# Kernel optimization log

Measured on AMD Instinct MI355X. Metric: run time of the kernel, lower is better.

## Reference

```python
import jax, jax.numpy as jnp
import numpy as np

KERNEL_MUL = 2.0
KERNEL_NUM = 5

def setup_inputs() -> dict:
    key = jax.random.key(0)
    k1, k2 = jax.random.split(key)
    source = jax.random.normal(k1, (4096, 256), dtype=jnp.float32)
    target = jax.random.normal(k2, (4096, 256), dtype=jnp.float32)
    return {"source": source, "target": target}

def reference(source, target):
    B = source.shape[0]
    total = jnp.concatenate([source, target], axis=0)           # [2N, D]
    n = total.shape[0]
    # pairwise squared L2 distances via expansion (same math as
    # ((total0 - total1)**2).sum(2) without the [2N,2N,D] intermediate)
    sq = jnp.sum(total * total, axis=-1)                         # [2N]
    l2 = jnp.maximum(sq[:, None] + sq[None, :] - 2.0 * (total @ total.T), 0.0)  # [2N,2N]
    # bandwidth from data mean of off-diagonal distances (detached in torch via .data)
    bandwidth = jax.lax.stop_gradient(jnp.sum(l2)) / (n * n - n)
    bandwidth = bandwidth / (KERNEL_MUL ** (KERNEL_NUM // 2))
    kernels = jnp.zeros_like(l2)
    for i in range(KERNEL_NUM):
        kernels = kernels + jnp.exp(-l2 / (bandwidth * (KERNEL_MUL ** i)))
    xx = kernels[:B, :B]
    yy = kernels[B:, B:]
    xy = kernels[:B, B:]
    yx = kernels[B:, :B]
    return jnp.mean(xx + yy - xy - yx)
```

## Files before the change

kernel.cpp:

```cpp
#include <hip/hip_runtime.h>


#define NROWS 8192
#define BHALF 4096
#define DDIM  256
#define TILE  128
#define BK    32
#define NTILE 64
#define NBLK  2080

typedef __attribute__((ext_vector_type(8))) short bf16x8;
typedef __attribute__((ext_vector_type(4))) float f32x4;
typedef __attribute__((ext_vector_type(2))) float f32x2;
typedef __attribute__((ext_vector_type(4))) unsigned short u16x4;

struct Ws {
  float coef;
  float Spart[256];
  float cpart[256][256];
  float sq[NROWS];
  float part[NBLK];
};

__device__ __forceinline__ unsigned short f2bf(float x) {
  unsigned int u = __builtin_bit_cast(unsigned int, x);
  return (unsigned short)((u + 0x7fffu + ((u >> 16) & 1u)) >> 16);
}

__device__ __forceinline__ const float* row_ptr(const float* src, const float* tgt, int i) {
  return (i < BHALF) ? (src + (size_t)i * DDIM) : (tgt + (size_t)(i - BHALF) * DDIM);
}

__global__ __launch_bounds__(256) void k_prep(const float* __restrict__ src,
                                              const float* __restrict__ tgt,
                                              Ws* __restrict__ ws,
                                              unsigned short* __restrict__ tb,
                                              int conv) {
  __shared__ float cls[4][256];
  __shared__ float sred[4];
  int tid = threadIdx.x, wave = tid >> 6, lane = tid & 63;
  int row0 = blockIdx.x * 32 + wave * 8;
  float c0 = 0.f, c1 = 0.f, c2 = 0.f, c3 = 0.f;
  float s[8];
  #pragma unroll
  for (int r = 0; r < 8; ++r) {
    const float4* rp = (const float4*)row_ptr(src, tgt, row0 + r);
    float4 x = rp[lane];
    if (conv) {
      u16x4 b = { f2bf(x.x), f2bf(x.y), f2bf(x.z), f2bf(x.w) };
      int rg = row0 + r;
      int t = rg >> 7, rl = rg & 127;
      int cg = lane >> 1;
      int k8 = cg >> 2, cwp = cg & 3;
      int slot = cwp ^ ((rl >> 1) & 3);
      *(u16x4*)&tb[((size_t)(t * 8 + k8) * 128 + rl) * 32 + slot * 8 + (lane & 1) * 4] = b;
    }
    c0 += x.x; c1 += x.y; c2 += x.z; c3 += x.w;
    s[r] = x.x * x.x + x.y * x.y + x.z * x.z + x.w * x.w;
  }
  #pragma unroll
  for (int off = 32; off > 0; off >>= 1) {
    #pragma unroll
    for (int r = 0; r < 8; ++r) s[r] += __shfl_xor(s[r], off);
  }
  if (lane == 0) {
    float Sw = 0.f;
    #pragma unroll
    for (int r = 0; r < 8; ++r) { ws->sq[row0 + r] = s[r]; Sw += s[r]; }
    sred[wave] = Sw;
  }
  cls[wave][lane * 4 + 0] = c0;
  cls[wave][lane * 4 + 1] = c1;
  cls[wave][lane * 4 + 2] = c2;
  cls[wave][lane * 4 + 3] = c3;
  __syncthreads();
  ws->cpart[blockIdx.x][tid] = cls[0][tid] + cls[1][tid] + cls[2][tid] + cls[3][tid];
  if (tid == 0) ws->Spart[blockIdx.x] = sred[0] + sred[1] + sred[2] + sred[3];
}

__global__ __launch_bounds__(256) void k_bw(Ws* __restrict__ ws) {
  __shared__ float redm[4], reds[4];
  int tid = threadIdx.x, wave = tid >> 6, lane = tid & 63;
  float mc = 0.f;
  for (int b0 = 0; b0 < 256; b0 += 16) {
    float v[16];
    #pragma unroll
    for (int j = 0; j < 16; ++j) v[j] = ws->cpart[b0 + j][tid];
    #pragma unroll
    for (int j = 0; j < 16; ++j) mc += v[j];
  }
  float p = mc * mc;
  float sp = ws->Spart[tid];
  #pragma unroll
  for (int off = 32; off > 0; off >>= 1) {
    p  += __shfl_xor(p, off);
    sp += __shfl_xor(sp, off);
  }
  if (lane == 0) { redm[wave] = p; reds[wave] = sp; }
  __syncthreads();
  if (tid == 0) {
    float msq = redm[0] + redm[1] + redm[2] + redm[3];
    float S   = reds[0] + reds[1] + reds[2] + reds[3];
    double n = (double)NROWS;
    double sum_l2 = 2.0 * n * (double)S - 2.0 * (double)msq;
    double bw = sum_l2 / (n * n - n) / 4.0;
    ws->coef = (float)(1.4426950408889634 / (16.0 * bw));
  }
}

__device__ __forceinline__ void stage32(const unsigned short* gA,
                                        const unsigned short* gB,
                                        unsigned short* lA, unsigned short* lB,
                                        int kcs) {
  #pragma unroll
  for (int t = 0; t < 2; ++t) {
    __builtin_amdgcn_global_load_lds(
        (const __attribute__((address_space(1))) void*)(gA + (size_t)kcs * 4096 + t * 512),
        (__attribute__((address_space(3))) void*)(lA + t * 512), 16, 0, 0);
    __builtin_amdgcn_global_load_lds(
        (const __attribute__((address_space(1))) void*)(gB + (size_t)kcs * 4096 + t * 512),
        (__attribute__((address_space(3))) void*)(lB + t * 512), 16, 0, 0);
  }
}

template <int FAST>
__global__ __launch_bounds__(256, 4) void k_main(const unsigned short* __restrict__ tb,
                                                 const float* __restrict__ src,
                                                 const float* __restrict__ tgt,
                                                 Ws* __restrict__ ws) {
  int bid = blockIdx.x;
  int idx = (bid & 7) * (NBLK / 8) + (bid >> 3);
  int ti = (int)((129.0 - sqrt(129.0 * 129.0 - 8.0 * (double)idx)) * 0.5);
  while (64 * (ti + 1) - ((ti + 1) * ti) / 2 <= idx) ++ti;
  while (64 * ti - (ti * (ti - 1)) / 2 > idx) --ti;
  int tj = ti + (idx - (64 * ti - (ti * (ti - 1)) / 2));

  __shared__ __align__(16) unsigned short As[2][TILE * BK];
  __shared__ __align__(16) unsigned short Bs[2][TILE * BK];
  __shared__ float wsum[4];

  int tid = threadIdx.x;
  int wave = tid >> 6, lane = tid & 63;
  int wm = wave >> 1, wn = wave & 1;
  int lr = lane & 15, q = lane >> 4;
  int Ib = ti * TILE, Jb = tj * TILE;

  f32x4 zero = {0.f, 0.f, 0.f, 0.f};
  f32x4 acc[4][4];
  #pragma unroll
  for (int m = 0; m < 4; ++m)
    #pragma unroll
    for (int n = 0; n < 4; ++n) acc[m][n] = zero;

  const int coff = ((q ^ ((lr >> 1) & 3)) << 3);

  if (FAST) {
    const unsigned short* gA = tb + (size_t)ti * 32768 + wave * 1024 + lane * 8;
    const unsigned short* gB = tb + (size_t)tj * 32768 + wave * 1024 + lane * 8;
    unsigned short* lA0 = &As[0][wave * 1024];
    unsigned short* lB0 = &Bs[0][wave * 1024];
    unsigned short* lA1 = &As[1][wave * 1024];
    unsigned short* lB1 = &Bs[1][wave * 1024];

    stage32(gA, gB, lA0, lB0, 0);
    #pragma unroll
    for (int kcs = 0; kcs < 8; ++kcs) {
      if (kcs < 7) {
        stage32(gA, gB, ((kcs + 1) & 1) ? lA1 : lA0,
                        ((kcs + 1) & 1) ? lB1 : lB0, kcs + 1);
        asm volatile("s_waitcnt vmcnt(4)" ::: "memory");
      } else {
        asm volatile("s_waitcnt vmcnt(0)" ::: "memory");
      }
      __builtin_amdgcn_s_barrier();
      const unsigned short* Ab = As[kcs & 1];
      const unsigned short* Bb = Bs[kcs & 1];
      bf16x8 af[4], bfr[4];
      #pragma unroll
      for (int m = 0; m < 4; ++m)
        af[m] = *(const bf16x8*)&Ab[(wm * 64 + m * 16 + lr) * BK + coff];
      #pragma unroll
      for (int n = 0; n < 4; ++n)
        bfr[n] = *(const bf16x8*)&Bb[(wn * 64 + n * 16 + lr) * BK + coff];
      #pragma unroll
      for (int m = 0; m < 4; ++m)
        #pragma unroll
        for (int n = 0; n < 4; ++n)
          acc[m][n] = __builtin_amdgcn_mfma_f32_16x16x32_bf16(af[m], bfr[n], acc[m][n], 0, 0, 0);
      __builtin_amdgcn_s_barrier();
    }
  } else {
    int row = tid >> 1, h = tid & 1;
    int fsw = (row >> 1) & 3;
    const float4* rpA = (const float4*)row_ptr(src, tgt, Ib + row);
    const float4* rpB = (const float4*)row_ptr(src, tgt, Jb + row);
    #pragma unroll
    for (int kcs = 0; kcs < 8; ++kcs) {
      if (kcs) __syncthreads();
      unsigned short* lA = As[kcs & 1];
      unsigned short* lB = Bs[kcs & 1];
      #pragma unroll
      for (int cc = 0; cc < 2; ++cc) {
        int c = h * 2 + cc;
        int slot = c ^ fsw;
        float4 v0 = rpA[kcs * 8 + c * 2], v1 = rpA[kcs * 8 + c * 2 + 1];
        u16x4 a0 = { f2bf(v0.x), f2bf(v0.y), f2bf(v0.z), f2bf(v0.w) };
        u16x4 a1 = { f2bf(v1.x), f2bf(v1.y), f2bf(v1.z), f2bf(v1.w) };
        *(u16x4*)&lA[row * BK + slot * 8]     = a0;
        *(u16x4*)&lA[row * BK + slot * 8 + 4] = a1;
        float4 w0 = rpB[kcs * 8 + c * 2], w1 = rpB[kcs * 8 + c * 2 + 1];
        u16x4 b0 = { f2bf(w0.x), f2bf(w0.y), f2bf(w0.z), f2bf(w0.w) };
        u16x4 b1 = { f2bf(w1.x), f2bf(w1.y), f2bf(w1.z), f2bf(w1.w) };
        *(u16x4*)&lB[row * BK + slot * 8]     = b0;
        *(u16x4*)&lB[row * BK + slot * 8 + 4] = b1;
      }
      __syncthreads();
      const unsigned short* Ab = As[kcs & 1];
      const unsigned short* Bb = Bs[kcs & 1];
      bf16x8 af[4], bfr[4];
      #pragma unroll
      for (int m = 0; m < 4; ++m)
        af[m] = *(const bf16x8*)&Ab[(wm * 64 + m * 16 + lr) * BK + coff];
      #pragma unroll
      for (int n = 0; n < 4; ++n)
        bfr[n] = *(const bf16x8*)&Bb[(wn * 64 + n * 16 + lr) * BK + coff];
      #pragma unroll
      for (int m = 0; m < 4; ++m)
        #pragma unroll
        for (int n = 0; n < 4; ++n)
          acc[m][n] = __builtin_amdgcn_mfma_f32_16x16x32_bf16(af[m], bfr[n], acc[m][n], 0, 0, 0);
    }
  }

  float coef = ws->coef;
  float coef2 = 2.f * coef;
  int ibase = Ib + wm * 64;
  int jbase = Jb + wn * 64;
  float nscj[4];
  f32x2 nsci01[4], nsci23[4];
  #pragma unroll
  for (int n = 0; n < 4; ++n) nscj[n] = -ws->sq[jbase + n * 16 + lr] * coef;
  #pragma unroll
  for (int m = 0; m < 4; ++m) {
    nsci01[m] = f32x2{ -ws->sq[ibase + m * 16 + q * 4 + 0] * coef,
                       -ws->sq[ibase + m * 16 + q * 4 + 1] * coef };
    nsci23[m] = f32x2{ -ws->sq[ibase + m * 16 + q * 4 + 2] * coef,
                       -ws->sq[ibase + m * 16 + q * 4 + 3] * coef };
  }

  const f32x2 c2v = { coef2, coef2 };
  f32x2 accA = {0.f, 0.f}, accB = {0.f, 0.f};
  f32x2 accC = {0.f, 0.f}, accD = {0.f, 0.f};
  #pragma unroll
  for (int m = 0; m < 4; ++m) {
    #pragma unroll
    for (int n = 0; n < 4; ++n) {
      f32x4 g = acc[m][n];
      f32x2 bj = { nscj[n], nscj[n] };
      f32x2 b01 = nsci01[m] + bj;
      f32x2 b23 = nsci23[m] + bj;
      f32x2 a01 = f32x2{g[0], g[1]} * c2v + b01;
      f32x2 a23 = f32x2{g[2], g[3]} * c2v + b23;
      f32x2 t0, t1;
      t0.x = __builtin_amdgcn_exp2f(a01.x); t0.y = __builtin_amdgcn_exp2f(a01.y);
      t1.x = __builtin_amdgcn_exp2f(a23.x); t1.y = __builtin_amdgcn_exp2f(a23.y);
      f32x2 p0 = t0 * t0, p1 = t1 * t1;
      f32x2 q0 = p0 * p0, q1 = p1 * p1;
      f32x2 r0v = q0 * q0, r1v = q1 * q1;
      accA += t0 + p0;
      accB += q0 + r0v;
      accA = r0v * r0v + accA;
      accC += t1 + p1;
      accD += q1 + r1v;
      accC = r1v * r1v + accC;
    }
  }
  float lsum = (accA.x + accA.y) + (accB.x + accB.y)
             + (accC.x + accC.y) + (accD.x + accD.y);
  #pragma unroll
  for (int off = 32; off > 0; off >>= 1) lsum += __shfl_xor(lsum, off);
  if (lane == 0) wsum[wave] = lsum;
  __syncthreads();
  if (tid == 0) {
    float tot = wsum[0] + wsum[1] + wsum[2] + wsum[3];
    float sA = (ti < 32) ? 1.f : -1.f;
    float sB = (tj < 32) ? 1.f : -1.f;
    float fac = sA * sB * ((ti == tj) ? 1.f : 2.f);
    ws->part[blockIdx.x] = fac * tot;
  }
}

__global__ __launch_bounds__(256) void k_final(const Ws* __restrict__ ws,
                                               float* __restrict__ out) {
  __shared__ double red[4];
  int tid = threadIdx.x, wave = tid >> 6, lane = tid & 63;
  double s = 0.0;
  for (int i = tid; i < NBLK; i += 256) s += (double)ws->part[i];
  #pragma unroll
  for (int off = 32; off > 0; off >>= 1) s += __shfl_xor(s, off);
  if (lane == 0) red[wave] = s;
  __syncthreads();
  if (tid == 0)
    out[0] = (float)((red[0] + red[1] + red[2] + red[3]) /
                     ((double)BHALF * (double)BHALF));
}

extern "C" void kernel_launch(void* const* d_in, const int* in_sizes, int n_in,
                              void* d_out, int out_size, void* d_ws, size_t ws_size,
                              hipStream_t stream) {
  const float* src = (const float*)d_in[0];
  const float* tgt = (const float*)d_in[1];
  Ws* ws = (Ws*)d_ws;
  float* out = (float*)d_out;

  size_t wsoff = (sizeof(Ws) + 255) & ~(size_t)255;
  size_t need = wsoff + (size_t)NROWS * DDIM * 2;
  bool fast = ws_size >= need;
  unsigned short* tb = fast ? (unsigned short*)((char*)d_ws + wsoff) : nullptr;

  hipLaunchKernelGGL(k_prep, dim3(256), dim3(256), 0, stream, src, tgt, ws, tb,
                     fast ? 1 : 0);
  hipLaunchKernelGGL(k_bw, dim3(1), dim3(256), 0, stream, ws);
  if (fast)
    hipLaunchKernelGGL((k_main<1>), dim3(NBLK), dim3(256), 0, stream, tb, src, tgt, ws);
  else
    hipLaunchKernelGGL((k_main<0>), dim3(NBLK), dim3(256), 0, stream, tb, src, tgt, ws);
  hipLaunchKernelGGL(k_final, dim3(1), dim3(256), 0, stream, ws, out);
}
```

Before: 101.5 us.

## Use 256x128 paired-row tiles with 512-thread blocks to share B loads

Replaces the 128x128 upper-triangular tile kernel with one whose blocks cover two vertically adjacent row tiles (256 rows) against one 128-column tile, using 8 waves. Each B-tile load is shared by two row tiles, cutting global-to-LDS traffic per output and the number of blocks. The triangular indexing now covers a band structure that computes some redundant lower-triangle work near the diagonal. The mapping of partial sums to slots is rewritten to match. The slow fallback is split into its own kernel.

Measured after the change: 99.95 us, median of 2. Within noise of the previous version (-1.5%).

```diff
diff --git a/kernel.cpp b/kernel.cpp
--- a/kernel.cpp
+++ b/kernel.cpp
@@ -4,10 +4,10 @@
 #define NROWS 8192
 #define BHALF 4096
 #define DDIM  256
-#define TILE  128
 #define BK    32
 #define NTILE 64
 #define NBLK  2080
+#define NBLK2 1056
 
 typedef __attribute__((ext_vector_type(8))) short bf16x8;
 typedef __attribute__((ext_vector_type(4))) float f32x4;
@@ -108,42 +108,39 @@
   }
 }
 
-__device__ __forceinline__ void stage32(const unsigned short* gA,
-                                        const unsigned short* gB,
-                                        unsigned short* lA, unsigned short* lB,
-                                        int kcs) {
-  #pragma unroll
-  for (int t = 0; t < 2; ++t) {
-    __builtin_amdgcn_global_load_lds(
-        (const __attribute__((address_space(1))) void*)(gA + (size_t)kcs * 4096 + t * 512),
-        (__attribute__((address_space(3))) void*)(lA + t * 512), 16, 0, 0);
-    __builtin_amdgcn_global_load_lds(
-        (const __attribute__((address_space(1))) void*)(gB + (size_t)kcs * 4096 + t * 512),
-        (__attribute__((address_space(3))) void*)(lB + t * 512), 16, 0, 0);
-  }
-}
-
-template <int FAST>
-__global__ __launch_bounds__(256, 4) void k_main(const unsigned short* __restrict__ tb,
-                                                 const float* __restrict__ src,
-                                                 const float* __restrict__ tgt,
-                                                 Ws* __restrict__ ws) {
+__device__ __forceinline__ void stage3(const unsigned short* gA,
+                                       const unsigned short* gB,
+                                       unsigned short* lA, unsigned short* lB,
+                                       int kcs) {
+  __builtin_amdgcn_global_load_lds(
+      (const __attribute__((address_space(1))) void*)(gA + (size_t)kcs * 4096),
+      (__attribute__((address_space(3))) void*)(lA), 16, 0, 0);
+  __builtin_amdgcn_global_load_lds(
+      (const __attribute__((address_space(1))) void*)(gA + (size_t)kcs * 4096 + 512),
+      (__attribute__((address_space(3))) void*)(lA + 512), 16, 0, 0);
+  __builtin_amdgcn_global_load_lds(
+      (const __attribute__((address_space(1))) void*)(gB + (size_t)kcs * 4096),
+      (__attribute__((address_space(3))) void*)(lB), 16, 0, 0);
+}
+
+__global__ __launch_bounds__(512, 4) void k_main2(const unsigned short* __restrict__ tb,
+                                                  Ws* __restrict__ ws) {
   int bid = blockIdx.x;
-  int idx = (bid & 7) * (NBLK / 8) + (bid >> 3);
-  int ti = (int)((129.0 - sqrt(129.0 * 129.0 - 8.0 * (double)idx)) * 0.5);
-  while (64 * (ti + 1) - ((ti + 1) * ti) / 2 <= idx) ++ti;
-  while (64 * ti - (ti * (ti - 1)) / 2 > idx) --ti;
-  int tj = ti + (idx - (64 * ti - (ti * (ti - 1)) / 2));
-
-  __shared__ __align__(16) unsigned short As[2][TILE * BK];
-  __shared__ __align__(16) unsigned short Bs[2][TILE * BK];
-  __shared__ float wsum[4];
+  int r = (bid & 7) * (NBLK2 / 8) + (bid >> 3);
+  int I = (int)((65.0 - sqrt(4225.0 - 4.0 * (double)r)) * 0.5);
+  while ((I + 1) * (65 - (I + 1)) <= r) ++I;
+  while (I * (65 - I) > r) --I;
+  int tj = 2 * I + (r - I * (65 - I));
+
+  __shared__ __align__(16) unsigned short As[2][256 * BK];
+  __shared__ __align__(16) unsigned short Bs[2][128 * BK];
+  __shared__ float wsum[8];
 
   int tid = threadIdx.x;
   int wave = tid >> 6, lane = tid & 63;
   int wm = wave >> 1, wn = wave & 1;
   int lr = lane & 15, q = lane >> 4;
-  int Ib = ti * TILE, Jb = tj * TILE;
+  const int coff = ((q ^ ((lr >> 1) & 3)) << 3);
 
   f32x4 zero = {0.f, 0.f, 0.f, 0.f};
   f32x4 acc[4][4];
@@ -152,90 +149,46 @@
     #pragma unroll
     for (int n = 0; n < 4; ++n) acc[m][n] = zero;
 
-  const int coff = ((q ^ ((lr >> 1) & 3)) << 3);
-
-  if (FAST) {
-    const unsigned short* gA = tb + (size_t)ti * 32768 + wave * 1024 + lane * 8;
-    const unsigned short* gB = tb + (size_t)tj * 32768 + wave * 1024 + lane * 8;
-    unsigned short* lA0 = &As[0][wave * 1024];
-    unsigned short* lB0 = &Bs[0][wave * 1024];
-    unsigned short* lA1 = &As[1][wave * 1024];
-    unsigned short* lB1 = &Bs[1][wave * 1024];
-
-    stage32(gA, gB, lA0, lB0, 0);
-    #pragma unroll
-    for (int kcs = 0; kcs < 8; ++kcs) {
-      if (kcs < 7) {
-        stage32(gA, gB, ((kcs + 1) & 1) ? lA1 : lA0,
-                        ((kcs + 1) & 1) ? lB1 : lB0, kcs + 1);
-        asm volatile("s_waitcnt vmcnt(4)" ::: "memory");
-      } else {
-        asm volatile("s_waitcnt vmcnt(0)" ::: "memory");
-      }
-      __builtin_amdgcn_s_barrier();
-      const unsigned short* Ab = As[kcs & 1];
-      const unsigned short* Bb = Bs[kcs & 1];
-      bf16x8 af[4], bfr[4];
-      #pragma unroll
-      for (int m = 0; m < 4; ++m)
-        af[m] = *(const bf16x8*)&Ab[(wm * 64 + m * 16 + lr) * BK + coff];
+  const unsigned short* gA = tb + (size_t)(2 * I + (wave >> 2)) * 32768
+                                + (32 * (wave & 3)) * 32 + lane * 8;
+  const unsigned short* gB = tb + (size_t)tj * 32768 + wave * 512 + lane * 8;
+  unsigned short* lA0 = &As[0][((wave >> 2) * 128 + 32 * (wave & 3)) * 32];
+  unsigned short* lB0 = &Bs[0][wave * 512];
+  unsigned short* lA1 = &As[1][((wave >> 2) * 128 + 32 * (wave & 3)) * 32];
+  unsigned short* lB1 = &Bs[1][wave * 512];
+
+  stage3(gA, gB, lA0, lB0, 0);
+  #pragma unroll
+  for (int kcs = 0; kcs < 8; ++kcs) {
+    if (kcs < 7) {
+      stage3(gA, gB, ((kcs + 1) & 1) ? lA1 : lA0,
+                     ((kcs + 1) & 1) ? lB1 : lB0, kcs + 1);
+      asm volatile("s_waitcnt vmcnt(3)" ::: "memory");
+    } else {
+      asm volatile("s_waitcnt vmcnt(0)" ::: "memory");
+    }
+    __builtin_amdgcn_s_barrier();
+    const unsigned short* Ab = As[kcs & 1];
+    const unsigned short* Bb = Bs[kcs & 1];
+    bf16x8 af[4], bfr[4];
+    #pragma unroll
+    for (int m = 0; m < 4; ++m)
+      af[m] = *(const bf16x8*)&Ab[(wm * 64 + m * 16 + lr) * BK + coff];
+    #pragma unroll
+    for (int n = 0; n < 4; ++n)
+      bfr[n] = *(const bf16x8*)&Bb[(wn * 64 + n * 16 + lr) * BK + coff];
+    #pragma unroll
+    for (int m = 0; m < 4; ++m)
       #pragma unroll
       for (int n = 0; n < 4; ++n)
-        bfr[n] = *(const bf16x8*)&Bb[(wn * 64 + n * 16 + lr) * BK + coff];
-      #pragma unroll
-      for (int m = 0; m < 4; ++m)
-        #pragma unroll
-        for (int n = 0; n < 4; ++n)
-          acc[m][n] = __builtin_amdgcn_mfma_f32_16x16x32_bf16(af[m], bfr[n], acc[m][n], 0, 0, 0);
-      __builtin_amdgcn_s_barrier();
-    }
-  } else {
-    int row = tid >> 1, h = tid & 1;
-    int fsw = (row >> 1) & 3;
-    const float4* rpA = (const float4*)row_ptr(src, tgt, Ib + row);
-    const float4* rpB = (const float4*)row_ptr(src, tgt, Jb + row);
-    #pragma unroll
-    for (int kcs = 0; kcs < 8; ++kcs) {
-      if (kcs) __syncthreads();
-      unsigned short* lA = As[kcs & 1];
-      unsigned short* lB = Bs[kcs & 1];
-      #pragma unroll
-      for (int cc = 0; cc < 2; ++cc) {
-        int c = h * 2 + cc;
-        int slot = c ^ fsw;
-        float4 v0 = rpA[kcs * 8 + c * 2], v1 = rpA[kcs * 8 + c * 2 + 1];
-        u16x4 a0 = { f2bf(v0.x), f2bf(v0.y), f2bf(v0.z), f2bf(v0.w) };
-        u16x4 a1 = { f2bf(v1.x), f2bf(v1.y), f2bf(v1.z), f2bf(v1.w) };
-        *(u16x4*)&lA[row * BK + slot * 8]     = a0;
-        *(u16x4*)&lA[row * BK + slot * 8 + 4] = a1;
-        float4 w0 = rpB[kcs * 8 + c * 2], w1 = rpB[kcs * 8 + c * 2 + 1];
-        u16x4 b0 = { f2bf(w0.x), f2bf(w0.y), f2bf(w0.z), f2bf(w0.w) };
-        u16x4 b1 = { f2bf(w1.x), f2bf(w1.y), f2bf(w1.z), f2bf(w1.w) };
-        *(u16x4*)&lB[row * BK + slot * 8]     = b0;
-        *(u16x4*)&lB[row * BK + slot * 8 + 4] = b1;
-      }
-      __syncthreads();
-      const unsigned short* Ab = As[kcs & 1];
-      const unsigned short* Bb = Bs[kcs & 1];
-      bf16x8 af[4], bfr[4];
-      #pragma unroll
-      for (int m = 0; m < 4; ++m)
-        af[m] = *(const bf16x8*)&Ab[(wm * 64 + m * 16 + lr) * BK + coff];
-      #pragma unroll
-      for (int n = 0; n < 4; ++n)
-        bfr[n] = *(const bf16x8*)&Bb[(wn * 64 + n * 16 + lr) * BK + coff];
-      #pragma unroll
-      for (int m = 0; m < 4; ++m)
-        #pragma unroll
-        for (int n = 0; n < 4; ++n)
-          acc[m][n] = __builtin_amdgcn_mfma_f32_16x16x32_bf16(af[m], bfr[n], acc[m][n], 0, 0, 0);
-    }
+        acc[m][n] = __builtin_amdgcn_mfma_f32_16x16x32_bf16(af[m], bfr[n], acc[m][n], 0, 0, 0);
+    __builtin_amdgcn_s_barrier();
   }
 
   float coef = ws->coef;
   float coef2 = 2.f * coef;
-  int ibase = Ib + wm * 64;
-  int jbase = Jb + wn * 64;
+  int ibase = I * 256 + wm * 64;
+  int jbase = tj * 128 + wn * 64;
   float nscj[4];
   f32x2 nsci01[4], nsci23[4];
   #pragma unroll
@@ -282,11 +235,150 @@
   if (lane == 0) wsum[wave] = lsum;
   __syncthreads();
   if (tid == 0) {
+    int t0 = 2 * I, t1 = 2 * I + 1;
+    float sband = (I < 16) ? 1.f : -1.f;
+    float sB = (tj < 32) ? 1.f : -1.f;
+    float topv = wsum[0] + wsum[1] + wsum[2] + wsum[3];
+    float botv = wsum[4] + wsum[5] + wsum[6] + wsum[7];
+    if (tj != t1) {
+      float fac = (tj == t0) ? 1.f : 2.f;
+      int rk = 64 * t0 - (t0 * (t0 - 1)) / 2 + (tj - t0);
+      ws->part[rk] = fac * sband * sB * topv;
+    }
+    {
+      float fac; int rk;
+      if (tj == t0)      { fac = 2.f; rk = 64 * t0 - (t0 * (t0 - 1)) / 2 + 1; }
+      else if (tj == t1) { fac = 1.f; rk = 64 * t1 - (t1 * (t1 - 1)) / 2; }
+      else               { fac = 2.f; rk = 64 * t1 - (t1 * (t1 - 1)) / 2 + (tj - t1); }
+      ws->part[rk] = fac * sband * sB * botv;
+    }
+  }
+}
+
+__global__ __launch_bounds__(256, 4) void k_main_slow(const float* __restrict__ src,
+                                                      const float* __restrict__ tgt,
+                                                      Ws* __restrict__ ws) {
+  int bid = blockIdx.x;
+  int idx = (bid & 7) * (NBLK / 8) + (bid >> 3);
+  int ti = (int)((129.0 - sqrt(129.0 * 129.0 - 8.0 * (double)idx)) * 0.5);
+  while (64 * (ti + 1) - ((ti + 1) * ti) / 2 <= idx) ++ti;
+  while (64 * ti - (ti * (ti - 1)) / 2 > idx) --ti;
+  int tj = ti + (idx - (64 * ti - (ti * (ti - 1)) / 2));
+
+  __shared__ __align__(16) unsigned short As[2][128 * BK];
+  __shared__ __align__(16) unsigned short Bs[2][128 * BK];
+  __shared__ float wsum[4];
+
+  int tid = threadIdx.x;
+  int wave = tid >> 6, lane = tid & 63;
+  int wm = wave >> 1, wn = wave & 1;
+  int lr = lane & 15, q = lane >> 4;
+  int Ib = ti * 128, Jb = tj * 128;
+
+  f32x4 zero = {0.f, 0.f, 0.f, 0.f};
+  f32x4 acc[4][4];
+  #pragma unroll
+  for (int m = 0; m < 4; ++m)
+    #pragma unroll
+    for (int n = 0; n < 4; ++n) acc[m][n] = zero;
+
+  const int coff = ((q ^ ((lr >> 1) & 3)) << 3);
+  int row = tid >> 1, h = tid & 1;
+  int fsw = (row >> 1) & 3;
+  const float4* rpA = (const float4*)row_ptr(src, tgt, Ib + row);
+  const float4* rpB = (const float4*)row_ptr(src, tgt, Jb + row);
+  #pragma unroll
+  for (int kcs = 0; kcs < 8; ++kcs) {
+    if (kcs) __syncthreads();
+    unsigned short* lA = As[kcs & 1];
+    unsigned short* lB = Bs[kcs & 1];
+    #pragma unroll
+    for (int cc = 0; cc < 2; ++cc) {
+      int cx = h * 2 + cc;
+      int slot = cx ^ fsw;
+      float4 v0 = rpA[kcs * 8 + cx * 2], v1 = rpA[kcs * 8 + cx * 2 + 1];
+      u16x4 a0 = { f2bf(v0.x), f2bf(v0.y), f2bf(v0.z), f2bf(v0.w) };
+      u16x4 a1 = { f2bf(v1.x), f2bf(v1.y), f2bf(v1.z), f2bf(v1.w) };
+      *(u16x4*)&lA[row * BK + slot * 8]     = a0;
+      *(u16x4*)&lA[row * BK + slot * 8 + 4] = a1;
+      float4 w0 = rpB[kcs * 8 + cx * 2], w1 = rpB[kcs * 8 + cx * 2 + 1];
+      u16x4 b0 = { f2bf(w0.x), f2bf(w0.y), f2bf(w0.z), f2bf(w0.w) };
+      u16x4 b1 = { f2bf(w1.x), f2bf(w1.y), f2bf(w1.z), f2bf(w1.w) };
+      *(u16x4*)&lB[row * BK + slot * 8]     = b0;
+      *(u16x4*)&lB[row * BK + slot * 8 + 4] = b1;
+    }
+    __syncthreads();
+    const unsigned short* Ab = As[kcs & 1];
+    const unsigned short* Bb = Bs[kcs & 1];
+    bf16x8 af[4], bfr[4];
+    #pragma unroll
+    for (int m = 0; m < 4; ++m)
+      af[m] = *(const bf16x8*)&Ab[(wm * 64 + m * 16 + lr) * BK + coff];
+    #pragma unroll
+    for (int n = 0; n < 4; ++n)
+      bfr[n] = *(const bf16x8*)&Bb[(wn * 64 + n * 16 + lr) * BK + coff];
+    #pragma unroll
+    for (int m = 0; m < 4; ++m)
+      #pragma unroll
+      for (int n = 0; n < 4; ++n)
+        acc[m][n] = __builtin_amdgcn_mfma_f32_16x16x32_bf16(af[m], bfr[n], acc[m][n], 0, 0, 0);
+  }
+
+  float coef = ws->coef;
+  float coef2 = 2.f * coef;
+  int ibase = Ib + wm * 64;
+  int jbase = Jb + wn * 64;
+  float nscj[4];
+  f32x2 nsci01[4], nsci23[4];
+  #pragma unroll
+  for (int n = 0; n < 4; ++n) nscj[n] = -ws->sq[jbase + n * 16 + lr] * coef;
+  #pragma unroll
+  for (int m = 0; m < 4; ++m) {
+    nsci01[m] = f32x2{ -ws->sq[ibase + m * 16 + q * 4 + 0] * coef,
+                       -ws->sq[ibase + m * 16 + q * 4 + 1] * coef };
+    nsci23[m] = f32x2{ -ws->sq[ibase + m * 16 + q * 4 + 2] * coef,
+                       -ws->sq[ibase + m * 16 + q * 4 + 3] * coef };
+  }
+  const f32x2 c2v = { coef2, coef2 };
+  f32x2 accA = {0.f, 0.f}, accB = {0.f, 0.f};
+  f32x2 accC = {0.f, 0.f}, accD = {0.f, 0.f};
+  #pragma unroll
+  for (int m = 0; m < 4; ++m) {
+    #pragma unroll
+    for (int n = 0; n < 4; ++n) {
+      f32x4 g = acc[m][n];
+      f32x2 bj = { nscj[n], nscj[n] };
+      f32x2 b01 = nsci01[m] + bj;
+      f32x2 b23 = nsci23[m] + bj;
+      f32x2 a01 = f32x2{g[0], g[1]} * c2v + b01;
+      f32x2 a23 = f32x2{g[2], g[3]} * c2v + b23;
+      f32x2 t0, t1;
+      t0.x = __builtin_amdgcn_exp2f(a01.x); t0.y = __builtin_amdgcn_exp2f(a01.y);
+      t1.x = __builtin_amdgcn_exp2f(a23.x); t1.y = __builtin_amdgcn_exp2f(a23.y);
+      f32x2 p0 = t0 * t0, p1 = t1 * t1;
+      f32x2 q0 = p0 * p0, q1 = p1 * p1;
+      f32x2 r0v = q0 * q0, r1v = q1 * q1;
+      accA += t0 + p0;
+      accB += q0 + r0v;
+      accA = r0v * r0v + accA;
+      accC += t1 + p1;
+      accD += q1 + r1v;
+      accC = r1v * r1v + accC;
+    }
+  }
+  float lsum = (accA.x + accA.y) + (accB.x + accB.y)
+             + (accC.x + accC.y) + (accD.x + accD.y);
+  #pragma unroll
+  for (int off = 32; off > 0; off >>= 1) lsum += __shfl_xor(lsum, off);
+  if (lane == 0) wsum[wave] = lsum;
+  __syncthreads();
+  if (tid == 0) {
     float tot = wsum[0] + wsum[1] + wsum[2] + wsum[3];
     float sA = (ti < 32) ? 1.f : -1.f;
     float sB = (tj < 32) ? 1.f : -1.f;
     float fac = sA * sB * ((ti == tj) ? 1.f : 2.f);
-    ws->part[blockIdx.x] = fac * tot;
+    int slot = 64 * ti - (ti * (ti - 1)) / 2 + (tj - ti);
+    ws->part[slot] = fac * tot;
   }
 }
 
@@ -322,8 +414,8 @@
                      fast ? 1 : 0);
   hipLaunchKernelGGL(k_bw, dim3(1), dim3(256), 0, stream, ws);
   if (fast)
-    hipLaunchKernelGGL((k_main<1>), dim3(NBLK), dim3(256), 0, stream, tb, src, tgt, ws);
+    hipLaunchKernelGGL(k_main2, dim3(NBLK2), dim3(512), 0, stream, tb, ws);
   else
-    hipLaunchKernelGGL((k_main<0>), dim3(NBLK), dim3(256), 0, stream, tb, src, tgt, ws);
+    hipLaunchKernelGGL(k_main_slow, dim3(NBLK), dim3(256), 0, stream, src, tgt, ws);
   hipLaunchKernelGGL(k_final, dim3(1), dim3(256), 0, stream, ws, out);
 }
```
